# Kernel tuning notes

Hardware: AMD Instinct MI355X
Metric: run time of the kernel (lower is better)

## Reference

```python
import jax, jax.numpy as jnp
import numpy as np
from jax import lax

B = 8192
DEPTH = 4096
SCALES = 3
FLT = 4  # db2 filter length

_DB2_DEC_LO = np.array([-0.12940952255092145, 0.22414386804185735, 0.836516303737469, 0.48296291314469025], dtype=np.float32)
_DB2_DEC_HI = np.array([-0.48296291314469025, 0.836516303737469, 0.22414386804185735, 0.12940952255092145], dtype=np.float32)


def _coeff_lens(depth, flen, scales):
    # mirrors pywt.dwt_coeff_len(n, flen, 'zero') = floor((n + flen - 1) / 2)
    lens = [depth]
    for _ in range(scales):
        lens.append((lens[-1] + flen - 1) // 2)
    lens = lens[1:]
    lens.append(lens[-1])
    return lens  # e.g. [2049, 1026, 514, 514]

WAVE_DEPTH = int(np.sum(_coeff_lens(DEPTH, FLT, SCALES)))  # 4103


def setup_inputs() -> dict:
    key = jax.random.key(0)
    ks = jax.random.split(key, 5)
    x = jax.random.normal(ks[0], (B, DEPTH), dtype=jnp.float32)
    diag_b = 1.0 + 0.1 * jax.random.normal(ks[1], (DEPTH,), dtype=jnp.float32)
    diag_g = 1.0 + 0.1 * jax.random.normal(ks[2], (WAVE_DEPTH,), dtype=jnp.float32)
    diag_s = 1.0 + 0.1 * jax.random.normal(ks[3], (DEPTH,), dtype=jnp.float32)
    dec_lo = jnp.asarray(_DB2_DEC_LO)
    dec_hi = jnp.asarray(_DB2_DEC_HI)
    rec_lo = dec_lo[::-1]
    rec_hi = dec_hi[::-1]
    perm_idx = jax.random.permutation(ks[4], WAVE_DEPTH).astype(jnp.int32)
    return {"x": x, "diag_b": diag_b, "diag_g": diag_g, "diag_s": diag_s,
            "dec_lo": dec_lo, "dec_hi": dec_hi, "rec_lo": rec_lo, "rec_hi": rec_hi,
            "perm_idx": perm_idx}


def _forward(x, diag_b, diag_g, diag_s, dec_lo, dec_hi, rec_lo, rec_hi, perm_idx):
    L = dec_lo.shape[0]
    lens = _coeff_lens(x.shape[-1], L, SCALES)
    # mul_b: diag(vec) matmul == elementwise column scale
    a = x * diag_b
    # multi-level analysis DWT with 'zero' padding: full convolution, keep odd indices
    w_dec = jnp.stack([dec_lo[::-1], dec_hi[::-1]])[:, None, :]  # [2,1,L] (flip: lax does corr)
    details = []
    for _ in range(SCALES):
        y = lax.conv_general_dilated(a[:, None, :], w_dec, (2,), [(L - 2, L - 1)],
                                     dimension_numbers=("NCH", "OIH", "NCH"))
        a, d = y[:, 0, :], y[:, 1, :]
        details.append(d)
    c = jnp.concatenate([a] + details[::-1], axis=-1)  # [B, WAVE_DEPTH], [cA_s, cD_s, ..., cD_1]
    # mul_p: permutation matmul == column gather
    c = c[:, perm_idx]
    # mul_g
    c = c * diag_g
    # coefficient slicing exactly as in the original forward (incl. its start-update rule)
    rev = lens[::-1]
    coeffs = []
    start = 0
    for s_i in range(SCALES + 1):
        stop = start + rev[s_i]
        coeffs.append(c[:, start:stop])
        start = lens[s_i]
    # multi-level reconstruction (idwt, zero mode): zero-upsample, full conv, trim L-2 per side
    a = coeffs[0]
    w_rec = jnp.stack([rec_lo[::-1], rec_hi[::-1]])[None, :, :]  # [1,2,L]
    for d in coeffs[1:]:
        if a.shape[-1] == d.shape[-1] + 1:  # pywt waverec odd-length trim
            a = a[:, :-1]
        xin = jnp.stack([a, d], axis=1)  # [B,2,la]
        a = lax.conv_general_dilated(xin, w_rec, (1,), [(1, 1)], lhs_dilation=(2,),
                                     dimension_numbers=("NCH", "OIH", "NCH"))[:, 0, :]
    # mul_s
    return a * diag_s


def reference(x, diag_b, diag_g, diag_s, dec_lo, dec_hi, rec_lo, rec_hi, perm_idx):
    return _forward(x, diag_b, diag_g, diag_s, dec_lo, dec_hi, rec_lo, rec_hi, perm_idx)
```

## Files before the change

kernel.cpp:

```cpp
#include <hip/hip_runtime.h>


#define NT 512

__global__ __launch_bounds__(NT, 8) void wavelet_fused(
    const float* __restrict__ x,
    const float* __restrict__ diag_b,
    const float* __restrict__ diag_g,
    const float* __restrict__ diag_s,
    const float* __restrict__ dec_lo,
    const float* __restrict__ dec_hi,
    const float* __restrict__ rec_lo,
    const float* __restrict__ rec_hi,
    const int*   __restrict__ perm_idx,
    float* __restrict__ out)
{
    __shared__ __align__(16) float rawA[3088];
    __shared__ __align__(16) float rawC[4112];
    float* const A1 = rawA + 4;
    float* const A2 = rawA + 2060;
    float* const R1 = rawA + 4;
    float* const Cc = rawC;

    const int tid = threadIdx.x;
    const long row = blockIdx.x;

    const float lo0=dec_lo[0], lo1=dec_lo[1], lo2=dec_lo[2], lo3=dec_lo[3];
    const float hi0=dec_hi[0], hi1=dec_hi[1], hi2=dec_hi[2], hi3=dec_hi[3];
    const float rl0=rec_lo[0], rl1=rec_lo[1], rl2=rec_lo[2], rl3=rec_lo[3];
    const float rh0=rec_hi[0], rh1=rec_hi[1], rh2=rec_hi[2], rh3=rec_hi[3];

    if (tid < 2) rawA[2 + tid]    = 0.0f;
    if (tid < 3) rawA[2053 + tid] = 0.0f;
    if (tid < 2) rawA[2058 + tid] = 0.0f;
    if (tid < 2) rawA[3086 + tid] = 0.0f;

    {
        const float* xr = x + row * 4096;
        float4 xv0 = *(const float4*)(xr + 8*tid);
        float4 xv1 = *(const float4*)(xr + 8*tid + 4);
        float4 bv0 = *(const float4*)(diag_b + 8*tid);
        float4 bv1 = *(const float4*)(diag_b + 8*tid + 4);
        float vm2 = 0.0f, vm1 = 0.0f;
        if (tid > 0) {
            float2 xm = *(const float2*)(xr + 8*tid - 2);
            float2 bm = *(const float2*)(diag_b + 8*tid - 2);
            vm2 = xm.x * bm.x; vm1 = xm.y * bm.y;
        }
        float v0 = xv0.x*bv0.x, v1 = xv0.y*bv0.y, v2 = xv0.z*bv0.z, v3 = xv0.w*bv0.w;
        float v4 = xv1.x*bv1.x, v5 = xv1.y*bv1.y, v6 = xv1.z*bv1.z, v7 = xv1.w*bv1.w;
        float4 av, dv;
        av.x = lo0*v1 + lo1*v0 + lo2*vm1 + lo3*vm2;
        dv.x = hi0*v1 + hi1*v0 + hi2*vm1 + hi3*vm2;
        av.y = lo0*v3 + lo1*v2 + lo2*v1 + lo3*v0;
        dv.y = hi0*v3 + hi1*v2 + hi2*v1 + hi3*v0;
        av.z = lo0*v5 + lo1*v4 + lo2*v3 + lo3*v2;
        dv.z = hi0*v5 + hi1*v4 + hi2*v3 + hi3*v2;
        av.w = lo0*v7 + lo1*v6 + lo2*v5 + lo3*v4;
        dv.w = hi0*v7 + hi1*v6 + hi2*v5 + hi3*v4;
        *(float4*)(A1 + 4*tid) = av;
        *(float4*)(Cc + 2056 + 4*tid) = dv;
        if (tid == 0) {
            float xa = xr[4094]*diag_b[4094], xb = xr[4095]*diag_b[4095];
            A1[2048]        = lo2*xb + lo3*xa;
            Cc[2056 + 2048] = hi2*xb + hi3*xa;
        }
    }
    __syncthreads();

    for (int p = tid; p < 513; p += NT) {
        float2 u0 = *(const float2*)(A1 + 4*p - 2);
        float4 u1 = *(const float4*)(A1 + 4*p);
        float2 ap, dp;
        ap.x = lo0*u1.y + lo1*u1.x + lo2*u0.y + lo3*u0.x;
        dp.x = hi0*u1.y + hi1*u1.x + hi2*u0.y + hi3*u0.x;
        ap.y = lo0*u1.w + lo1*u1.z + lo2*u1.y + lo3*u1.x;
        dp.y = hi0*u1.w + hi1*u1.z + hi2*u1.y + hi3*u1.x;
        *(float2*)(A2 + 2*p)        = ap;
        *(float2*)(Cc + 1028 + 2*p) = dp;
    }
    __syncthreads();

    for (int p = tid; p < 257; p += NT) {
        float2 u0 = *(const float2*)(A2 + 4*p - 2);
        float4 u1 = *(const float4*)(A2 + 4*p);
        float2 ap, dp;
        ap.x = lo0*u1.y + lo1*u1.x + lo2*u0.y + lo3*u0.x;
        dp.x = hi0*u1.y + hi1*u1.x + hi2*u0.y + hi3*u0.x;
        ap.y = lo0*u1.w + lo1*u1.z + lo2*u1.y + lo3*u1.x;
        dp.y = hi0*u1.w + hi1*u1.z + hi2*u1.y + hi3*u1.x;
        *(float2*)(Cc + 2*p)       = ap;
        *(float2*)(Cc + 514 + 2*p) = dp;
    }
    __syncthreads();

    auto CPj = [&](int j) -> float {
        return Cc[j + (j >= 2054 ? 2 : 0)];
    };
    auto CP = [&](int i) -> float {
        return CPj(perm_idx[i]) * diag_g[i];
    };

    for (int k = tid; k < 513; k += NT) {
        float a0 = CP(k),        a1v = CP(k + 1);
        float d0 = CP(2049 + k), d1v = CP(2050 + k);
        float2 w;
        w.x = rl2*a0 + rl0*a1v + rh2*d0 + rh0*d1v;
        w.y = rl3*a0 + rl1*a1v + rh3*d0 + rh1*d1v;
        *(float2*)(R1 + 2*k) = w;
    }
    __syncthreads();

    {
        const int u = tid;
        float2 q01 = *(const float2*)(R1 + 2*u);
        float2 q23 = *(const float2*)(R1 + 2*u + 2);
        int2   pe0 = *(const int2*)(perm_idx + 1026 + 2*u);
        int2   pe1 = *(const int2*)(perm_idx + 1028 + 2*u);
        float2 ge0 = *(const float2*)(diag_g + 1026 + 2*u);
        float2 ge1 = *(const float2*)(diag_g + 1028 + 2*u);
        float e0 = CPj(pe0.x) * ge0.x, e1 = CPj(pe0.y) * ge0.y;
        float e2 = CPj(pe1.x) * ge1.x, e3 = CPj(pe1.y) * ge1.y;
        float s0  = rl2*q01.x + rl0*q01.y + rh2*e0 + rh0*e1;
        float s1v = rl3*q01.x + rl1*q01.y + rh3*e0 + rh1*e1;
        float s2v = rl2*q01.y + rl0*q23.x + rh2*e1 + rh0*e2;
        float s3v = rl3*q01.y + rl1*q23.x + rh3*e1 + rh1*e2;
        float s4  = rl2*q23.x + rl0*q23.y + rh2*e2 + rh0*e3;
        int2   pf0 = *(const int2*)(perm_idx + 514 + 4*u);
        int2   pf1 = *(const int2*)(perm_idx + 516 + 4*u);
        int    pf2 = perm_idx[518 + 4*u];
        float2 gf0 = *(const float2*)(diag_g + 514 + 4*u);
        float2 gf1 = *(const float2*)(diag_g + 516 + 4*u);
        float  gf2 = diag_g[518 + 4*u];
        float f0 = CPj(pf0.x) * gf0.x, f1 = CPj(pf0.y) * gf0.y;
        float f2 = CPj(pf1.x) * gf1.x, f3 = CPj(pf1.y) * gf1.y;
        float f4 = CPj(pf2)   * gf2;
        float4 ss0 = ((const float4*)diag_s)[2*u];
        float4 ss1 = ((const float4*)diag_s)[2*u + 1];
        float4 o0, o1;
        o0.x = (rl2*s0  + rl0*s1v + rh2*f0 + rh0*f1) * ss0.x;
        o0.y = (rl3*s0  + rl1*s1v + rh3*f0 + rh1*f1) * ss0.y;
        o0.z = (rl2*s1v + rl0*s2v + rh2*f1 + rh0*f2) * ss0.z;
        o0.w = (rl3*s1v + rl1*s2v + rh3*f1 + rh1*f2) * ss0.w;
        o1.x = (rl2*s2v + rl0*s3v + rh2*f2 + rh0*f3) * ss1.x;
        o1.y = (rl3*s2v + rl1*s3v + rh3*f2 + rh1*f3) * ss1.y;
        o1.z = (rl2*s3v + rl0*s4  + rh2*f3 + rh0*f4) * ss1.z;
        o1.w = (rl3*s3v + rl1*s4  + rh3*f3 + rh1*f4) * ss1.w;
        float4* outr = (float4*)(out + row * 4096);
        outr[2*u]     = o0;
        outr[2*u + 1] = o1;
    }
}

extern "C" void kernel_launch(void* const* d_in, const int* in_sizes, int n_in,
                              void* d_out, int out_size, void* d_ws, size_t ws_size,
                              hipStream_t stream) {
    const float* x       = (const float*)d_in[0];
    const float* diag_b  = (const float*)d_in[1];
    const float* diag_g  = (const float*)d_in[2];
    const float* diag_s  = (const float*)d_in[3];
    const float* dec_lo  = (const float*)d_in[4];
    const float* dec_hi  = (const float*)d_in[5];
    const float* rec_lo  = (const float*)d_in[6];
    const float* rec_hi  = (const float*)d_in[7];
    const int*   perm    = (const int*)d_in[8];
    float* out = (float*)d_out;

    const int B = in_sizes[0] / 4096;
    wavelet_fused<<<B, NT, 0, stream>>>(
        x, diag_b, diag_g, diag_s, dec_lo, dec_hi, rec_lo, rec_hi, perm, out);
}
```

Measured before the change: 269.5 us.

## Prefetch perm/diag vectors at kernel start and materialize permuted coefficients in LDS

Loads perm_idx, diag_g and diag_s into registers with vectorized loads at kernel entry, so their global latency overlaps the analysis stages. Adds a stage that gathers and scales all used permuted coefficients once into a shared buffer, which the reconstruction stages then read. This replaces the scattered per-use global index loads and the duplicated gathers of the old path. The cost is one more barrier, extra live registers across the whole kernel that may lower occupancy, and R1 moving into the rawC buffer.

```diff
diff --git a/kernel.cpp b/kernel.cpp
--- a/kernel.cpp
+++ b/kernel.cpp
@@ -19,11 +19,24 @@
     __shared__ __align__(16) float rawC[4112];
     float* const A1 = rawA + 4;
     float* const A2 = rawA + 2060;
-    float* const R1 = rawA + 4;
+    float* const P  = rawA;
     float* const Cc = rawC;
+    float* const R1 = rawC;
 
     const int tid = threadIdx.x;
     const long row = blockIdx.x;
+
+    int4   pq0 = ((const int4*)perm_idx)[tid];
+    float4 gq0 = ((const float4*)diag_g)[tid];
+    int4   pq1; float4 gq1;
+    if (tid < 128) {
+        pq1 = ((const int4*)perm_idx)[512 + tid];
+        gq1 = ((const float4*)diag_g)[512 + tid];
+    }
+    int pt = 0; float gt = 0.0f;
+    if (tid < 3) { pt = perm_idx[2560 + tid]; gt = diag_g[2560 + tid]; }
+    float4 sv0 = ((const float4*)diag_s)[2*tid];
+    float4 sv1 = ((const float4*)diag_s)[2*tid + 1];
 
     const float lo0=dec_lo[0], lo1=dec_lo[1], lo2=dec_lo[2], lo3=dec_lo[3];
     const float hi0=dec_hi[0], hi1=dec_hi[1], hi2=dec_hi[2], hi3=dec_hi[3];
@@ -94,20 +107,37 @@
     }
     __syncthreads();
 
-    auto CPj = [&](int j) -> float {
-        return Cc[j + (j >= 2054 ? 2 : 0)];
-    };
-    auto CP = [&](int i) -> float {
-        return CPj(perm_idx[i]) * diag_g[i];
-    };
+    {
+        float4 cv;
+        cv.x = Cc[pq0.x + (pq0.x >= 2054 ? 2 : 0)] * gq0.x;
+        cv.y = Cc[pq0.y + (pq0.y >= 2054 ? 2 : 0)] * gq0.y;
+        cv.z = Cc[pq0.z + (pq0.z >= 2054 ? 2 : 0)] * gq0.z;
+        cv.w = Cc[pq0.w + (pq0.w >= 2054 ? 2 : 0)] * gq0.w;
+        *(float4*)(P + 4*tid) = cv;
+        if (tid < 128) {
+            float4 cw;
+            cw.x = Cc[pq1.x + (pq1.x >= 2054 ? 2 : 0)] * gq1.x;
+            cw.y = Cc[pq1.y + (pq1.y >= 2054 ? 2 : 0)] * gq1.y;
+            cw.z = Cc[pq1.z + (pq1.z >= 2054 ? 2 : 0)] * gq1.z;
+            cw.w = Cc[pq1.w + (pq1.w >= 2054 ? 2 : 0)] * gq1.w;
+            *(float4*)(P + 2048 + 4*tid) = cw;
+        }
+        if (tid < 3)  P[2560 + tid] = Cc[pt + (pt >= 2054 ? 2 : 0)] * gt;
+        if (tid == 3) P[2563] = 0.0f;
+    }
+    __syncthreads();
 
-    for (int k = tid; k < 513; k += NT) {
-        float a0 = CP(k),        a1v = CP(k + 1);
-        float d0 = CP(2049 + k), d1v = CP(2050 + k);
-        float2 w;
-        w.x = rl2*a0 + rl0*a1v + rh2*d0 + rh0*d1v;
-        w.y = rl3*a0 + rl1*a1v + rh3*d0 + rh1*d1v;
-        *(float2*)(R1 + 2*k) = w;
+    if (tid < 257) {
+        int p0 = 2 * tid;
+        float a0v = P[p0],        a1v = P[p0 + 1],    a2v = P[p0 + 2];
+        float d0v = P[2049 + p0], d1v = P[2050 + p0], d2v = P[2051 + p0];
+        float4 w;
+        w.x = rl2*a0v + rl0*a1v + rh2*d0v + rh0*d1v;
+        w.y = rl3*a0v + rl1*a1v + rh3*d0v + rh1*d1v;
+        w.z = rl2*a1v + rl0*a2v + rh2*d1v + rh0*d2v;
+        w.w = rl3*a1v + rl1*a2v + rh3*d1v + rh1*d2v;
+        if (tid < 256) *(float4*)(R1 + 4*tid) = w;
+        else           { R1[1024] = w.x; R1[1025] = w.y; }
     }
     __syncthreads();
 
@@ -115,37 +145,27 @@
         const int u = tid;
         float2 q01 = *(const float2*)(R1 + 2*u);
         float2 q23 = *(const float2*)(R1 + 2*u + 2);
-        int2   pe0 = *(const int2*)(perm_idx + 1026 + 2*u);
-        int2   pe1 = *(const int2*)(perm_idx + 1028 + 2*u);
-        float2 ge0 = *(const float2*)(diag_g + 1026 + 2*u);
-        float2 ge1 = *(const float2*)(diag_g + 1028 + 2*u);
-        float e0 = CPj(pe0.x) * ge0.x, e1 = CPj(pe0.y) * ge0.y;
-        float e2 = CPj(pe1.x) * ge1.x, e3 = CPj(pe1.y) * ge1.y;
+        float2 ea  = *(const float2*)(P + 1026 + 2*u);
+        float2 eb  = *(const float2*)(P + 1028 + 2*u);
+        float e0 = ea.x, e1 = ea.y, e2 = eb.x, e3 = eb.y;
         float s0  = rl2*q01.x + rl0*q01.y + rh2*e0 + rh0*e1;
         float s1v = rl3*q01.x + rl1*q01.y + rh3*e0 + rh1*e1;
         float s2v = rl2*q01.y + rl0*q23.x + rh2*e1 + rh0*e2;
         float s3v = rl3*q01.y + rl1*q23.x + rh3*e1 + rh1*e2;
         float s4  = rl2*q23.x + rl0*q23.y + rh2*e2 + rh0*e3;
-        int2   pf0 = *(const int2*)(perm_idx + 514 + 4*u);
-        int2   pf1 = *(const int2*)(perm_idx + 516 + 4*u);
-        int    pf2 = perm_idx[518 + 4*u];
-        float2 gf0 = *(const float2*)(diag_g + 514 + 4*u);
-        float2 gf1 = *(const float2*)(diag_g + 516 + 4*u);
-        float  gf2 = diag_g[518 + 4*u];
-        float f0 = CPj(pf0.x) * gf0.x, f1 = CPj(pf0.y) * gf0.y;
-        float f2 = CPj(pf1.x) * gf1.x, f3 = CPj(pf1.y) * gf1.y;
-        float f4 = CPj(pf2)   * gf2;
-        float4 ss0 = ((const float4*)diag_s)[2*u];
-        float4 ss1 = ((const float4*)diag_s)[2*u + 1];
+        float2 fa = *(const float2*)(P + 514 + 4*u);
+        float2 fb = *(const float2*)(P + 516 + 4*u);
+        float  f4 = P[518 + 4*u];
+        float f0 = fa.x, f1 = fa.y, f2 = fb.x, f3 = fb.y;
         float4 o0, o1;
-        o0.x = (rl2*s0  + rl0*s1v + rh2*f0 + rh0*f1) * ss0.x;
-        o0.y = (rl3*s0  + rl1*s1v + rh3*f0 + rh1*f1) * ss0.y;
-        o0.z = (rl2*s1v + rl0*s2v + rh2*f1 + rh0*f2) * ss0.z;
-        o0.w = (rl3*s1v + rl1*s2v + rh3*f1 + rh1*f2) * ss0.w;
-        o1.x = (rl2*s2v + rl0*s3v + rh2*f2 + rh0*f3) * ss1.x;
-        o1.y = (rl3*s2v + rl1*s3v + rh3*f2 + rh1*f3) * ss1.y;
-        o1.z = (rl2*s3v + rl0*s4  + rh2*f3 + rh0*f4) * ss1.z;
-        o1.w = (rl3*s3v + rl1*s4  + rh3*f3 + rh1*f4) * ss1.w;
+        o0.x = (rl2*s0  + rl0*s1v + rh2*f0 + rh0*f1) * sv0.x;
+        o0.y = (rl3*s0  + rl1*s1v + rh3*f0 + rh1*f1) * sv0.y;
+        o0.z = (rl2*s1v + rl0*s2v + rh2*f1 + rh0*f2) * sv0.z;
+        o0.w = (rl3*s1v + rl1*s2v + rh3*f1 + rh1*f2) * sv0.w;
+        o1.x = (rl2*s2v + rl0*s3v + rh2*f2 + rh0*f3) * sv1.x;
+        o1.y = (rl3*s2v + rl1*s3v + rh3*f2 + rh1*f3) * sv1.y;
+        o1.z = (rl2*s3v + rl0*s4  + rh2*f3 + rh0*f4) * sv1.z;
+        o1.w = (rl3*s3v + rl1*s4  + rh3*f3 + rh1*f4) * sv1.w;
         float4* outr = (float4*)(out + row * 4096);
         outr[2*u]     = o0;
         outr[2*u + 1] = o1;
```

Measured after the change: 261.3 us. -3.0%, faster.

## Process four rows per block with prefetch and precomputed permuted coefficient buffer

Applied to the files above, without the earlier changes.

Each block now handles four rows in sequence, loading diag_b once and prefetching the next row's input into registers while the current row is being processed. The permutation gather and diag_g scaling are done once into a shared buffer P, so the reconstruction stages read contiguous shared memory instead of repeating gathers. The first reconstruction level is folded into the final stage, which removes one barrier. The costs are more registers and fewer blocks (B/4), which may reduce parallelism, and it assumes B is divisible by four.

```diff
diff --git a/kernel.cpp b/kernel.cpp
--- a/kernel.cpp
+++ b/kernel.cpp
@@ -1,7 +1,8 @@
 #include <hip/hip_runtime.h>
 
 
-#define NT 512
+#define NT   512
+#define ROWS 4
 
 __global__ __launch_bounds__(NT, 8) void wavelet_fused(
     const float* __restrict__ x,
@@ -19,137 +20,164 @@
     __shared__ __align__(16) float rawC[4112];
     float* const A1 = rawA + 4;
     float* const A2 = rawA + 2060;
-    float* const R1 = rawA + 4;
+    float* const P  = rawA;
     float* const Cc = rawC;
 
     const int tid = threadIdx.x;
-    const long row = blockIdx.x;
+    const long row0 = (long)blockIdx.x * ROWS;
 
     const float lo0=dec_lo[0], lo1=dec_lo[1], lo2=dec_lo[2], lo3=dec_lo[3];
     const float hi0=dec_hi[0], hi1=dec_hi[1], hi2=dec_hi[2], hi3=dec_hi[3];
     const float rl0=rec_lo[0], rl1=rec_lo[1], rl2=rec_lo[2], rl3=rec_lo[3];
     const float rh0=rec_hi[0], rh1=rec_hi[1], rh2=rec_hi[2], rh3=rec_hi[3];
 
-    if (tid < 2) rawA[2 + tid]    = 0.0f;
-    if (tid < 3) rawA[2053 + tid] = 0.0f;
-    if (tid < 2) rawA[2058 + tid] = 0.0f;
+    float4 bv0 = *(const float4*)(diag_b + 8*tid);
+    float4 bv1 = *(const float4*)(diag_b + 8*tid + 4);
+    float2 bm; bm.x = 0.0f; bm.y = 0.0f;
+    if (tid > 0) bm = *(const float2*)(diag_b + 8*tid - 2);
+
     if (tid < 2) rawA[3086 + tid] = 0.0f;
 
-    {
-        const float* xr = x + row * 4096;
-        float4 xv0 = *(const float4*)(xr + 8*tid);
-        float4 xv1 = *(const float4*)(xr + 8*tid + 4);
-        float4 bv0 = *(const float4*)(diag_b + 8*tid);
-        float4 bv1 = *(const float4*)(diag_b + 8*tid + 4);
-        float vm2 = 0.0f, vm1 = 0.0f;
-        if (tid > 0) {
-            float2 xm = *(const float2*)(xr + 8*tid - 2);
-            float2 bm = *(const float2*)(diag_b + 8*tid - 2);
-            vm2 = xm.x * bm.x; vm1 = xm.y * bm.y;
-        }
-        float v0 = xv0.x*bv0.x, v1 = xv0.y*bv0.y, v2 = xv0.z*bv0.z, v3 = xv0.w*bv0.w;
-        float v4 = xv1.x*bv1.x, v5 = xv1.y*bv1.y, v6 = xv1.z*bv1.z, v7 = xv1.w*bv1.w;
-        float4 av, dv;
-        av.x = lo0*v1 + lo1*v0 + lo2*vm1 + lo3*vm2;
-        dv.x = hi0*v1 + hi1*v0 + hi2*vm1 + hi3*vm2;
-        av.y = lo0*v3 + lo1*v2 + lo2*v1 + lo3*v0;
-        dv.y = hi0*v3 + hi1*v2 + hi2*v1 + hi3*v0;
-        av.z = lo0*v5 + lo1*v4 + lo2*v3 + lo3*v2;
-        dv.z = hi0*v5 + hi1*v4 + hi2*v3 + hi3*v2;
-        av.w = lo0*v7 + lo1*v6 + lo2*v5 + lo3*v4;
-        dv.w = hi0*v7 + hi1*v6 + hi2*v5 + hi3*v4;
-        *(float4*)(A1 + 4*tid) = av;
-        *(float4*)(Cc + 2056 + 4*tid) = dv;
-        if (tid == 0) {
-            float xa = xr[4094]*diag_b[4094], xb = xr[4095]*diag_b[4095];
-            A1[2048]        = lo2*xb + lo3*xa;
-            Cc[2056 + 2048] = hi2*xb + hi3*xa;
-        }
-    }
+#define LOADX(ROW, XV0, XV1, XM) do {                                   \
+        const float* xr_ = x + (long)(ROW) * 4096;                      \
+        XV0 = *(const float4*)(xr_ + 8*tid);                            \
+        XV1 = *(const float4*)(xr_ + 8*tid + 4);                        \
+        XM.x = 0.0f; XM.y = 0.0f;                                       \
+        if (tid > 0) XM = *(const float2*)(xr_ + 8*tid - 2);            \
+    } while (0)
+
+#define ROW_BODY(ROW, XV0, XV1, XM, PF) {                               \
+     \
+    if (tid < 2) rawA[2 + tid]    = 0.0f;                               \
+    if (tid < 3) rawA[2053 + tid] = 0.0f;                               \
+    if (tid < 2) rawA[2058 + tid] = 0.0f;                               \
+            \
+    {                                                                   \
+        float v0 = XV0.x*bv0.x, v1 = XV0.y*bv0.y,                       \
+              v2 = XV0.z*bv0.z, v3 = XV0.w*bv0.w;                       \
+        float v4 = XV1.x*bv1.x, v5 = XV1.y*bv1.y,                       \
+              v6 = XV1.z*bv1.z, v7 = XV1.w*bv1.w;                       \
+        float vm2 = XM.x*bm.x, vm1 = XM.y*bm.y;                         \
+        float4 av, dv;                                                  \
+        av.x = lo0*v1 + lo1*v0 + lo2*vm1 + lo3*vm2;                     \
+        dv.x = hi0*v1 + hi1*v0 + hi2*vm1 + hi3*vm2;                     \
+        av.y = lo0*v3 + lo1*v2 + lo2*v1 + lo3*v0;                       \
+        dv.y = hi0*v3 + hi1*v2 + hi2*v1 + hi3*v0;                       \
+        av.z = lo0*v5 + lo1*v4 + lo2*v3 + lo3*v2;                       \
+        dv.z = hi0*v5 + hi1*v4 + hi2*v3 + hi3*v2;                       \
+        av.w = lo0*v7 + lo1*v6 + lo2*v5 + lo3*v4;                       \
+        dv.w = hi0*v7 + hi1*v6 + hi2*v5 + hi3*v4;                       \
+        *(float4*)(A1 + 4*tid) = av;                                    \
+        *(float4*)(Cc + 2056 + 4*tid) = dv;                             \
+        if (tid == 511) {     \
+            A1[2048]        = lo2*v7 + lo3*v6;                          \
+            Cc[2056 + 2048] = hi2*v7 + hi3*v6;                          \
+        }                                                               \
+    }                                                                   \
+    PF;          \
+    __syncthreads();                                                    \
+                         \
+    for (int p = tid; p < 513; p += NT) {                               \
+        float2 u0 = *(const float2*)(A1 + 4*p - 2);                     \
+        float4 u1 = *(const float4*)(A1 + 4*p);                         \
+        float2 ap, dp;                                                  \
+        ap.x = lo0*u1.y + lo1*u1.x + lo2*u0.y + lo3*u0.x;               \
+        dp.x = hi0*u1.y + hi1*u1.x + hi2*u0.y + hi3*u0.x;               \
+        ap.y = lo0*u1.w + lo1*u1.z + lo2*u1.y + lo3*u1.x;               \
+        dp.y = hi0*u1.w + hi1*u1.z + hi2*u1.y + hi3*u1.x;               \
+        *(float2*)(A2 + 2*p)        = ap;                               \
+        *(float2*)(Cc + 1028 + 2*p) = dp;                               \
+    }                                                                   \
+    __syncthreads();                                                    \
+             \
+    for (int p = tid; p < 257; p += NT) {                               \
+        float2 u0 = *(const float2*)(A2 + 4*p - 2);                     \
+        float4 u1 = *(const float4*)(A2 + 4*p);                         \
+        float2 ap, dp;                                                  \
+        ap.x = lo0*u1.y + lo1*u1.x + lo2*u0.y + lo3*u0.x;               \
+        dp.x = hi0*u1.y + hi1*u1.x + hi2*u0.y + hi3*u0.x;               \
+        ap.y = lo0*u1.w + lo1*u1.z + lo2*u1.y + lo3*u1.x;               \
+        dp.y = hi0*u1.w + hi1*u1.z + hi2*u1.y + hi3*u1.x;               \
+        *(float2*)(Cc + 2*p)       = ap;                                \
+        *(float2*)(Cc + 514 + 2*p) = dp;                                \
+    }                                                                   \
+    __syncthreads();                                                    \
+     \
+    {                                                                   \
+        int4   pj = ((const int4*)perm_idx)[tid];                       \
+        float4 g4 = ((const float4*)diag_g)[tid];                       \
+        float4 cv;                                                      \
+        cv.x = Cc[pj.x + (pj.x >= 2054 ? 2 : 0)] * g4.x;                \
+        cv.y = Cc[pj.y + (pj.y >= 2054 ? 2 : 0)] * g4.y;                \
+        cv.z = Cc[pj.z + (pj.z >= 2054 ? 2 : 0)] * g4.z;                \
+        cv.w = Cc[pj.w + (pj.w >= 2054 ? 2 : 0)] * g4.w;                \
+        *(float4*)(P + 4*tid) = cv;                                     \
+        if (tid < 128) {                                                \
+            int4   pk = ((const int4*)perm_idx)[512 + tid];             \
+            float4 gk = ((const float4*)diag_g)[512 + tid];             \
+            float4 cw;                                                  \
+            cw.x = Cc[pk.x + (pk.x >= 2054 ? 2 : 0)] * gk.x;            \
+            cw.y = Cc[pk.y + (pk.y >= 2054 ? 2 : 0)] * gk.y;            \
+            cw.z = Cc[pk.z + (pk.z >= 2054 ? 2 : 0)] * gk.z;            \
+            cw.w = Cc[pk.w + (pk.w >= 2054 ? 2 : 0)] * gk.w;            \
+            *(float4*)(P + 2048 + 4*tid) = cw;                          \
+        }                                                               \
+        if (tid < 3) {                                                  \
+            int pt = perm_idx[2560 + tid];                              \
+            P[2560 + tid] = Cc[pt + (pt >= 2054 ? 2 : 0)] * diag_g[2560 + tid]; \
+        }                                                               \
+    }                                                                   \
+    __syncthreads();                                                    \
+     \
+    {                                                                   \
+        const int u = tid;                                              \
+        float a0 = P[u], a1v = P[u + 1], a2v = P[u + 2];                \
+        float b0 = P[2049 + u], b1 = P[2050 + u], b2 = P[2051 + u];     \
+        float r10 = rl2*a0  + rl0*a1v + rh2*b0 + rh0*b1;                \
+        float r11 = rl3*a0  + rl1*a1v + rh3*b0 + rh1*b1;                \
+        float r12 = rl2*a1v + rl0*a2v + rh2*b1 + rh0*b2;                \
+        float r13 = rl3*a1v + rl1*a2v + rh3*b1 + rh1*b2;                \
+        float2 ea = *(const float2*)(P + 1026 + 2*u);                   \
+        float2 eb = *(const float2*)(P + 1028 + 2*u);                   \
+        float s0  = rl2*r10 + rl0*r11 + rh2*ea.x + rh0*ea.y;            \
+        float s1v = rl3*r10 + rl1*r11 + rh3*ea.x + rh1*ea.y;            \
+        float s2v = rl2*r11 + rl0*r12 + rh2*ea.y + rh0*eb.x;            \
+        float s3v = rl3*r11 + rl1*r12 + rh3*ea.y + rh1*eb.x;            \
+        float s4  = rl2*r12 + rl0*r13 + rh2*eb.x + rh0*eb.y;            \
+        float2 fa = *(const float2*)(P + 514 + 4*u);                    \
+        float2 fb = *(const float2*)(P + 516 + 4*u);                    \
+        float  f4 = P[518 + 4*u];                                       \
+        float4 sv0 = ((const float4*)diag_s)[2*u];                      \
+        float4 sv1 = ((const float4*)diag_s)[2*u + 1];                  \
+        float4 o0, o1;                                                  \
+        o0.x = (rl2*s0  + rl0*s1v + rh2*fa.x + rh0*fa.y) * sv0.x;       \
+        o0.y = (rl3*s0  + rl1*s1v + rh3*fa.x + rh1*fa.y) * sv0.y;       \
+        o0.z = (rl2*s1v + rl0*s2v + rh2*fa.y + rh0*fb.x) * sv0.z;       \
+        o0.w = (rl3*s1v + rl1*s2v + rh3*fa.y + rh1*fb.x) * sv0.w;       \
+        o1.x = (rl2*s2v + rl0*s3v + rh2*fb.x + rh0*fb.y) * sv1.x;       \
+        o1.y = (rl3*s2v + rl1*s3v + rh3*fb.x + rh1*fb.y) * sv1.y;       \
+        o1.z = (rl2*s3v + rl0*s4  + rh2*fb.y + rh0*f4  ) * sv1.z;       \
+        o1.w = (rl3*s3v + rl1*s4  + rh3*fb.y + rh1*f4  ) * sv1.w;       \
+        float4* outr = (float4*)(out + (long)(ROW) * 4096);             \
+        outr[2*u]     = o0;                                             \
+        outr[2*u + 1] = o1;                                             \
+    }                                                                   \
+}
+
+    float4 xA0, xA1; float2 xAm;
+    float4 xB0, xB1; float2 xBm;
+    LOADX(row0, xA0, xA1, xAm);
+
+    ROW_BODY(row0 + 0, xA0, xA1, xAm, LOADX(row0 + 1, xB0, xB1, xBm));
     __syncthreads();
-
-    for (int p = tid; p < 513; p += NT) {
-        float2 u0 = *(const float2*)(A1 + 4*p - 2);
-        float4 u1 = *(const float4*)(A1 + 4*p);
-        float2 ap, dp;
-        ap.x = lo0*u1.y + lo1*u1.x + lo2*u0.y + lo3*u0.x;
-        dp.x = hi0*u1.y + hi1*u1.x + hi2*u0.y + hi3*u0.x;
-        ap.y = lo0*u1.w + lo1*u1.z + lo2*u1.y + lo3*u1.x;
-        dp.y = hi0*u1.w + hi1*u1.z + hi2*u1.y + hi3*u1.x;
-        *(float2*)(A2 + 2*p)        = ap;
-        *(float2*)(Cc + 1028 + 2*p) = dp;
-    }
+    ROW_BODY(row0 + 1, xB0, xB1, xBm, LOADX(row0 + 2, xA0, xA1, xAm));
     __syncthreads();
-
-    for (int p = tid; p < 257; p += NT) {
-        float2 u0 = *(const float2*)(A2 + 4*p - 2);
-        float4 u1 = *(const float4*)(A2 + 4*p);
-        float2 ap, dp;
-        ap.x = lo0*u1.y + lo1*u1.x + lo2*u0.y + lo3*u0.x;
-        dp.x = hi0*u1.y + hi1*u1.x + hi2*u0.y + hi3*u0.x;
-        ap.y = lo0*u1.w + lo1*u1.z + lo2*u1.y + lo3*u1.x;
-        dp.y = hi0*u1.w + hi1*u1.z + hi2*u1.y + hi3*u1.x;
-        *(float2*)(Cc + 2*p)       = ap;
-        *(float2*)(Cc + 514 + 2*p) = dp;
-    }
+    ROW_BODY(row0 + 2, xA0, xA1, xAm, LOADX(row0 + 3, xB0, xB1, xBm));
     __syncthreads();
-
-    auto CPj = [&](int j) -> float {
-        return Cc[j + (j >= 2054 ? 2 : 0)];
-    };
-    auto CP = [&](int i) -> float {
-        return CPj(perm_idx[i]) * diag_g[i];
-    };
-
-    for (int k = tid; k < 513; k += NT) {
-        float a0 = CP(k),        a1v = CP(k + 1);
-        float d0 = CP(2049 + k), d1v = CP(2050 + k);
-        float2 w;
-        w.x = rl2*a0 + rl0*a1v + rh2*d0 + rh0*d1v;
-        w.y = rl3*a0 + rl1*a1v + rh3*d0 + rh1*d1v;
-        *(float2*)(R1 + 2*k) = w;
-    }
-    __syncthreads();
-
-    {
-        const int u = tid;
-        float2 q01 = *(const float2*)(R1 + 2*u);
-        float2 q23 = *(const float2*)(R1 + 2*u + 2);
-        int2   pe0 = *(const int2*)(perm_idx + 1026 + 2*u);
-        int2   pe1 = *(const int2*)(perm_idx + 1028 + 2*u);
-        float2 ge0 = *(const float2*)(diag_g + 1026 + 2*u);
-        float2 ge1 = *(const float2*)(diag_g + 1028 + 2*u);
-        float e0 = CPj(pe0.x) * ge0.x, e1 = CPj(pe0.y) * ge0.y;
-        float e2 = CPj(pe1.x) * ge1.x, e3 = CPj(pe1.y) * ge1.y;
-        float s0  = rl2*q01.x + rl0*q01.y + rh2*e0 + rh0*e1;
-        float s1v = rl3*q01.x + rl1*q01.y + rh3*e0 + rh1*e1;
-        float s2v = rl2*q01.y + rl0*q23.x + rh2*e1 + rh0*e2;
-        float s3v = rl3*q01.y + rl1*q23.x + rh3*e1 + rh1*e2;
-        float s4  = rl2*q23.x + rl0*q23.y + rh2*e2 + rh0*e3;
-        int2   pf0 = *(const int2*)(perm_idx + 514 + 4*u);
-        int2   pf1 = *(const int2*)(perm_idx + 516 + 4*u);
-        int    pf2 = perm_idx[518 + 4*u];
-        float2 gf0 = *(const float2*)(diag_g + 514 + 4*u);
-        float2 gf1 = *(const float2*)(diag_g + 516 + 4*u);
-        float  gf2 = diag_g[518 + 4*u];
-        float f0 = CPj(pf0.x) * gf0.x, f1 = CPj(pf0.y) * gf0.y;
-        float f2 = CPj(pf1.x) * gf1.x, f3 = CPj(pf1.y) * gf1.y;
-        float f4 = CPj(pf2)   * gf2;
-        float4 ss0 = ((const float4*)diag_s)[2*u];
-        float4 ss1 = ((const float4*)diag_s)[2*u + 1];
-        float4 o0, o1;
-        o0.x = (rl2*s0  + rl0*s1v + rh2*f0 + rh0*f1) * ss0.x;
-        o0.y = (rl3*s0  + rl1*s1v + rh3*f0 + rh1*f1) * ss0.y;
-        o0.z = (rl2*s1v + rl0*s2v + rh2*f1 + rh0*f2) * ss0.z;
-        o0.w = (rl3*s1v + rl1*s2v + rh3*f1 + rh1*f2) * ss0.w;
-        o1.x = (rl2*s2v + rl0*s3v + rh2*f2 + rh0*f3) * ss1.x;
-        o1.y = (rl3*s2v + rl1*s3v + rh3*f2 + rh1*f3) * ss1.y;
-        o1.z = (rl2*s3v + rl0*s4  + rh2*f3 + rh0*f4) * ss1.z;
-        o1.w = (rl3*s3v + rl1*s4  + rh3*f3 + rh1*f4) * ss1.w;
-        float4* outr = (float4*)(out + row * 4096);
-        outr[2*u]     = o0;
-        outr[2*u + 1] = o1;
-    }
+    ROW_BODY(row0 + 3, xB0, xB1, xBm, ((void)0));
+
+#undef ROW_BODY
+#undef LOADX
 }
 
 extern "C" void kernel_launch(void* const* d_in, const int* in_sizes, int n_in,
@@ -167,6 +195,6 @@
     float* out = (float*)d_out;
 
     const int B = in_sizes[0] / 4096;
-    wavelet_fused<<<B, NT, 0, stream>>>(
+    wavelet_fused<<<B / ROWS, NT, 0, stream>>>(
         x, diag_b, diag_g, diag_s, dec_lo, dec_hi, rec_lo, rec_hi, perm, out);
 }
```

Measured after the change: 265.0 us. Within noise of the previous version (-1.7%).
